# Optimization experiments

Measured on AMD Instinct MI355X. Metric: run time of the kernel, lower is better.

The kernel has to match this reference:

```python
import jax, jax.numpy as jnp
import numpy as np

B, C, H, W = 8, 256, 128, 128


def _bilinear_sample(img, gx, gy):
    """F.grid_sample(bilinear, padding_mode='zeros', align_corners=False).
    img: [B,C,H,W]; gx, gy: [B,H,W] normalized coords in [-1,1].
    Returns [B,C,H,W]."""
    Bi, Ci, Hi, Wi = img.shape
    ix = ((gx + 1.0) * Wi - 1.0) * 0.5  # pixel x coord
    iy = ((gy + 1.0) * Hi - 1.0) * 0.5  # pixel y coord
    ix0 = jnp.floor(ix)
    iy0 = jnp.floor(iy)
    wx1 = ix - ix0
    wy1 = iy - iy0
    bidx = jnp.arange(Bi)[:, None, None]

    def gather(iyf, ixf):
        valid = (ixf >= 0) & (ixf < Wi) & (iyf >= 0) & (iyf < Hi)
        iyc = jnp.clip(iyf, 0, Hi - 1).astype(jnp.int32)
        ixc = jnp.clip(ixf, 0, Wi - 1).astype(jnp.int32)
        v = img[bidx, :, iyc, ixc]  # [B,H,W,C]
        return jnp.where(valid[..., None], v, jnp.zeros((), img.dtype))

    v00 = gather(iy0, ix0)
    v01 = gather(iy0, ix0 + 1)
    v10 = gather(iy0 + 1, ix0)
    v11 = gather(iy0 + 1, ix0 + 1)
    w00 = ((1.0 - wy1) * (1.0 - wx1))[..., None]
    w01 = ((1.0 - wy1) * wx1)[..., None]
    w10 = (wy1 * (1.0 - wx1))[..., None]
    w11 = (wy1 * wx1)[..., None]
    out = v00 * w00 + v01 * w01 + v10 * w10 + v11 * w11  # [B,H,W,C]
    return out.transpose(0, 3, 1, 2)


def setup_inputs() -> dict:
    key = jax.random.key(0)
    ks = jax.random.split(key, 7)
    s = 1.0 / np.sqrt(C)
    return {
        "x": jax.random.normal(ks[0], (B, C, H, W), jnp.float32),
        "w_dw": jax.random.normal(ks[1], (C,), jnp.float32) * s,        # depthwise 1x1, no bias
        "w_off": jax.random.normal(ks[2], (2, C), jnp.float32) * s,     # offset 1x1 conv C->2
        "b_off": jax.random.normal(ks[3], (2,), jnp.float32) * 0.1,
        "w_pc": jax.random.normal(ks[4], (C, C), jnp.float32) * s,      # pointwise 1x1, no bias
        "w_W": jax.random.normal(ks[5], (C, C), jnp.float32) * s,       # residual-merge 1x1 conv
        "b_W": jax.random.normal(ks[6], (C,), jnp.float32) * 0.1,
    }


def reference(x, w_dw, w_off, b_off, w_pc, w_W, b_W):
    # offset = tanh(Conv1x1(x)) -> one shared (dx, dy) field (group == inplanes)
    offset = jnp.tanh(jnp.einsum('oc,bchw->bohw', w_off, x) + b_off[None, :, None, None])
    # depthwise 1x1 conv (bias=False) == per-channel scale
    dw = x * w_dw[None, :, None, None]
    # base normalized grid: X varies along W, Y along H (np.meshgrid convention)
    gx_base = jnp.linspace(-1.0, 1.0, W)[None, None, :]  # [1,1,W]
    gy_base = jnp.linspace(-1.0, 1.0, H)[None, :, None]  # [1,H,1]
    gx = jnp.clip(gx_base + offset[:, 0], -1.0, 1.0)  # [B,H,W]
    gy = jnp.clip(gy_base + offset[:, 1], -1.0, 1.0)
    sampled = _bilinear_sample(dw, gx, gy)             # [B,C,H,W]
    out = jnp.einsum('oc,bchw->bohw', w_pc, sampled)   # pointwise conv
    out = jnp.einsum('oc,bchw->bohw', w_W, out) + b_W[None, :, None, None]
    return out + x
```

## Files before the change

kernel.cpp:

```cpp
#include <hip/hip_runtime.h>
#include <hip/hip_bf16.h>

#define Bn 8
#define Cn 256
#define Hn 128
#define Wn 128
#define HWn (Hn * Wn)

typedef __attribute__((ext_vector_type(8))) short bfrag8;
typedef __attribute__((ext_vector_type(8))) unsigned short u16x8;
typedef __attribute__((ext_vector_type(4))) float f32x4;
typedef __attribute__((ext_vector_type(4))) unsigned int u32x4;

__device__ __forceinline__ float bf2f(unsigned short u) {
    unsigned int v = ((unsigned int)u) << 16;
    return __builtin_bit_cast(float, v);
}
__device__ __forceinline__ unsigned short f2bf(float f) {
    unsigned int u = __builtin_bit_cast(unsigned int, f);
    unsigned int lsb = (u >> 16) & 1u;
    u += 0x7fffu + lsb;
    return (unsigned short)(u >> 16);
}

__device__ __forceinline__ void load_lds16(const void* g, void* l) {
    __builtin_amdgcn_global_load_lds(
        (const __attribute__((address_space(1))) unsigned int*)g,
        (__attribute__((address_space(3))) unsigned int*)l,
        16, 0, 0);
}

__global__ __launch_bounds__(256)
void build_wcomb(const float* __restrict__ w_dw,
                 const float* __restrict__ w_pc,
                 const float* __restrict__ w_W,
                 unsigned short* __restrict__ wfrag) {
    const int o = blockIdx.x;
    const int c = threadIdx.x;
    float acc = 0.f;
#pragma unroll 8
    for (int k = 0; k < Cn; ++k)
        acc = fmaf(w_W[o * Cn + k], w_pc[k * Cn + c], acc);
    const int ob = o >> 4, lr = o & 15;
    const int ks = c >> 5, lg = (c & 31) >> 3, e = c & 7;
    const int lane = (lg << 4) + lr;
    wfrag[((((ob << 3) + ks) << 6) + lane) * 8 + e] = f2bf(acc * w_dw[c]);
}

__global__ __launch_bounds__(512, 2)
void prep_kernel(const float* __restrict__ x,
                 const float* __restrict__ w_off,
                 const float* __restrict__ b_off,
                 unsigned short* __restrict__ x_t,
                 float2* __restrict__ coords) {
    __shared__ __align__(16) char tile[256 * 256];
    __shared__ float wo[2][8][33];
    const int t = threadIdx.x;
    const int lane = t & 63;
    const int wv = t >> 6;
    int blk = blockIdx.x;
    blk = ((blk & 7) << 8) | (blk >> 3);
    const int b = blk >> 8;
    const int p0 = (blk & 255) << 6;
    const float* xp = x + ((size_t)b * Cn) * HWn + p0;

    {
        const int which = t >> 8, c = t & 255;
        wo[which][c >> 5][c & 31] = w_off[(which << 8) + c];
    }

    {
        const int r = lane >> 4;
        const int q = lane & 15;
#pragma unroll
        for (int i = 0; i < 8; ++i) {
            const int cbase = (wv << 5) + (i << 2);
            const int c = cbase + r;
            const int swz = (c ^ (c >> 4)) & 15;
            const float* src = xp + (size_t)c * HWn + ((q ^ swz) << 2);
            load_lds16(src, tile + (cbase << 8));
        }
    }
    __syncthreads();

    {
        const int pp = t >> 3;
        const int g = t & 7;
        float s0 = 0.f, s1 = 0.f;
        u16x8 res[4];
#pragma unroll
        for (int s = 0; s < 32; ++s) {
            const int c = (g << 5) + s;
            const int swz = (c ^ (c >> 4)) & 15;
            const int byte = (c << 8) + ((((pp >> 2) ^ swz)) << 4) + ((pp & 3) << 2);
            float v = *reinterpret_cast<const float*>(tile + byte);
            s0 = fmaf(v, wo[0][g][s], s0);
            s1 = fmaf(v, wo[1][g][s], s1);
            res[s >> 3][s & 7] = f2bf(v);
        }

        s0 += __shfl_xor(s0, 1); s0 += __shfl_xor(s0, 2); s0 += __shfl_xor(s0, 4);
        s1 += __shfl_xor(s1, 1); s1 += __shfl_xor(s1, 2); s1 += __shfl_xor(s1, 4);
        if (g == 0) {
            float o0 = tanhf(s0 + b_off[0]);
            float o1 = tanhf(s1 + b_off[1]);
            int p = p0 + pp;
            int yy = p >> 7, xx = p & 127;
            float gx = fminf(fmaxf(-1.f + xx * (2.f / 127.f) + o0, -1.f), 1.f);
            float gy = fminf(fmaxf(-1.f + yy * (2.f / 127.f) + o1, -1.f), 1.f);
            coords[(size_t)b * HWn + p] = make_float2(gx * 64.f + 63.5f, gy * 64.f + 63.5f);
        }

        unsigned short* dst = x_t + ((size_t)(b * HWn + p0 + pp)) * Cn + (g << 5);
#pragma unroll
        for (int j = 0; j < 4; ++j)
            *reinterpret_cast<u32x4*>(dst + (j << 3)) = __builtin_bit_cast(u32x4, res[j]);
    }
}

__global__ __launch_bounds__(512, 2)
void main_kernel(const float* __restrict__ x,
                 const float* __restrict__ b_W,
                 const unsigned short* __restrict__ x_t,
                 const float2* __restrict__ coords,
                 const unsigned short* __restrict__ wfrag,
                 float* __restrict__ out) {
    __shared__ __align__(16) char As[4][32 * 512];
    __shared__ __align__(16) float4 wts[32];
    const int t = threadIdx.x;
    const int lane = t & 63;
    const int wid = t >> 6;
    int blk = blockIdx.x;
    blk = ((blk & 7) << 9) | (blk >> 3);
    const int b = blk >> 9;
    const int p0 = (blk & 511) << 5;
    const size_t pixbase = (size_t)b * HWn + p0;
    const unsigned short* xtb = x_t + (size_t)b * HWn * Cn;

    if (t < 32) {
        float2 co = coords[pixbase + t];
        float ix = co.x, iy = co.y;
        float fx = floorf(ix), fy = floorf(iy);
        int ix0 = (int)fx, iy0 = (int)fy;
        float wx1 = ix - fx, wy1 = iy - fy;
        float wx0 = 1.f - wx1, wy0 = 1.f - wy1;
        bool vx0 = (ix0 >= 0) && (ix0 < Wn);
        bool vx1 = (ix0 >= -1) && (ix0 < Wn - 1);
        bool vy0 = (iy0 >= 0) && (iy0 < Hn);
        bool vy1 = (iy0 >= -1) && (iy0 < Hn - 1);
        float4 w;
        w.x = (vy0 && vx0) ? wy0 * wx0 : 0.f;
        w.y = (vy0 && vx1) ? wy0 * wx1 : 0.f;
        w.z = (vy1 && vx0) ? wy1 * wx0 : 0.f;
        w.w = (vy1 && vx1) ? wy1 * wx1 : 0.f;
        wts[t] = w;
    }

    {
        const int hp = lane >> 5;
        const int j = lane & 31;
        float2 co[2];
#pragma unroll
        for (int i = 0; i < 2; ++i)
            co[i] = coords[pixbase + (wid << 2) + (i << 1) + hp];

#pragma unroll
        for (int i = 0; i < 2; ++i) {
            const int p = (wid << 2) + (i << 1);
            const int px = p + hp;
            float ix = co[i].x, iy = co[i].y;
            int ix0 = (int)floorf(ix), iy0 = (int)floorf(iy);
            int cx0 = min(max(ix0, 0), Wn - 1), cx1 = min(max(ix0 + 1, 0), Wn - 1);
            int cy0 = min(max(iy0, 0), Hn - 1), cy1 = min(max(iy0 + 1, 0), Hn - 1);
            const int gch = (j ^ (px & 15)) << 3;
            const unsigned short* s00 = xtb + (size_t)(cy0 * Wn + cx0) * Cn + gch;
            const unsigned short* s01 = xtb + (size_t)(cy0 * Wn + cx1) * Cn + gch;
            const unsigned short* s10 = xtb + (size_t)(cy1 * Wn + cx0) * Cn + gch;
            const unsigned short* s11 = xtb + (size_t)(cy1 * Wn + cx1) * Cn + gch;
            load_lds16(s00, &As[0][p << 9]);
            load_lds16(s01, &As[1][p << 9]);
            load_lds16(s10, &As[2][p << 9]);
            load_lds16(s11, &As[3][p << 9]);
        }
    }
    __syncthreads();

    {
        const int px = t >> 4;
        const float4 w = wts[px];
#pragma unroll
        for (int q = 0; q < 2; ++q) {
            const int kc = (t & 15) + (q << 4);
            const int off = (px << 9) + ((kc ^ (px & 15)) << 4);
            u16x8 c00 = *reinterpret_cast<const u16x8*>(&As[0][off]);
            u16x8 c01 = *reinterpret_cast<const u16x8*>(&As[1][off]);
            u16x8 c10 = *reinterpret_cast<const u16x8*>(&As[2][off]);
            u16x8 c11 = *reinterpret_cast<const u16x8*>(&As[3][off]);
            u16x8 res;
#pragma unroll
            for (int e = 0; e < 8; ++e) {
                float r = w.x * bf2f(c00[e]) + w.y * bf2f(c01[e])
                        + w.z * bf2f(c10[e]) + w.w * bf2f(c11[e]);
                res[e] = f2bf(r);
            }
            *reinterpret_cast<u16x8*>(&As[0][off]) = res;
        }
    }
    __syncthreads();

    const int lr = lane & 15;
    const int lg = lane >> 4;
    f32x4 acc[2][2];
#pragma unroll
    for (int m = 0; m < 2; ++m)
#pragma unroll
        for (int n = 0; n < 2; ++n)
            acc[m][n] = (f32x4){0.f, 0.f, 0.f, 0.f};

#pragma unroll
    for (int ks = 0; ks < 8; ++ks) {
        bfrag8 a[2], bb[2];
        const int kc = (ks << 2) + lg;
#pragma unroll
        for (int n = 0; n < 2; ++n) {
            const int pr = (n << 4) + lr;
            const int off = (pr << 9) + ((kc ^ (pr & 15)) << 4);
            bb[n] = *reinterpret_cast<const bfrag8*>(&As[0][off]);
        }
#pragma unroll
        for (int m = 0; m < 2; ++m) {
            const int ob = (wid << 1) + m;
            const unsigned short* src = wfrag + ((((ob << 3) + ks) << 6) + lane) * 8;
            a[m] = *reinterpret_cast<const bfrag8*>(src);
        }
#pragma unroll
        for (int m = 0; m < 2; ++m)
#pragma unroll
            for (int n = 0; n < 2; ++n)
                acc[m][n] = __builtin_amdgcn_mfma_f32_16x16x32_bf16(a[m], bb[n], acc[m][n], 0, 0, 0);
    }

#pragma unroll
    for (int m = 0; m < 2; ++m) {
#pragma unroll
        for (int r = 0; r < 4; ++r) {
            int o = (wid << 5) + (m << 4) + (lg << 2) + r;
            float bw = b_W[o];
            size_t rowbase = ((size_t)b * Cn + o) * HWn + p0;
#pragma unroll
            for (int n = 0; n < 2; ++n) {
                size_t idx = rowbase + (n << 4) + lr;
                __builtin_nontemporal_store(acc[m][n][r] + bw + x[idx], &out[idx]);
            }
        }
    }
}

extern "C" void kernel_launch(void* const* d_in, const int* in_sizes, int n_in,
                              void* d_out, int out_size, void* d_ws, size_t ws_size,
                              hipStream_t stream) {
    const float* x     = (const float*)d_in[0];
    const float* w_dw  = (const float*)d_in[1];
    const float* w_off = (const float*)d_in[2];
    const float* b_off = (const float*)d_in[3];
    const float* w_pc  = (const float*)d_in[4];
    const float* w_W   = (const float*)d_in[5];
    const float* b_W   = (const float*)d_in[6];
    float* out = (float*)d_out;

    char* ws = (char*)d_ws;
    unsigned short* x_t   = (unsigned short*)ws;
    float2* coords        = (float2*)(ws + 67108864);
    unsigned short* wcomb = (unsigned short*)(ws + 67108864 + 1048576);

    build_wcomb<<<dim3(256), dim3(256), 0, stream>>>(w_dw, w_pc, w_W, wcomb);
    prep_kernel<<<dim3(2048), dim3(512), 0, stream>>>(x, w_off, b_off, x_t, coords);
    main_kernel<<<dim3(4096), dim3(512), 0, stream>>>(x, b_W, x_t, coords, wcomb, out);
}
```

Measured before the change: 121.3 us.

## Restructure prep kernel into double-buffered channel-slice pipeline over 512 pixels

The prep kernel now has each block handle 512 pixels, with one pixel per thread, and walks the 256 channels in eight 32-channel slices. Slice loads go into two LDS buffers so the next slice's global-to-LDS copy overlaps the current slice's offset-conv accumulation and bf16 transpose store. This removes the shuffle reduction and the swizzled tile reads. In exchange the grid shrinks from 2048 to 256 blocks with one block per CU, which may leave CUs underused and lower the memory parallelism available to this bandwidth-bound step.

```diff
diff --git a/kernel.cpp b/kernel.cpp
--- a/kernel.cpp
+++ b/kernel.cpp
@@ -47,75 +47,70 @@
     wfrag[((((ob << 3) + ks) << 6) + lane) * 8 + e] = f2bf(acc * w_dw[c]);
 }
 
-__global__ __launch_bounds__(512, 2)
+__global__ __launch_bounds__(512, 1)
 void prep_kernel(const float* __restrict__ x,
                  const float* __restrict__ w_off,
                  const float* __restrict__ b_off,
                  unsigned short* __restrict__ x_t,
                  float2* __restrict__ coords) {
-    __shared__ __align__(16) char tile[256 * 256];
-    __shared__ float wo[2][8][33];
+    __shared__ __align__(16) char bufs[2][32 * 512 * 4];
+    __shared__ float wo[2][256];
     const int t = threadIdx.x;
     const int lane = t & 63;
     const int wv = t >> 6;
     int blk = blockIdx.x;
-    blk = ((blk & 7) << 8) | (blk >> 3);
-    const int b = blk >> 8;
-    const int p0 = (blk & 255) << 6;
+    blk = ((blk & 7) << 5) | (blk >> 3);
+    const int b = blk >> 5;
+    const int p0 = (blk & 31) << 9;
     const float* xp = x + ((size_t)b * Cn) * HWn + p0;
 
-    {
-        const int which = t >> 8, c = t & 255;
-        wo[which][c >> 5][c & 31] = w_off[(which << 8) + c];
-    }
-
-    {
-        const int r = lane >> 4;
-        const int q = lane & 15;
-#pragma unroll
-        for (int i = 0; i < 8; ++i) {
-            const int cbase = (wv << 5) + (i << 2);
-            const int c = cbase + r;
-            const int swz = (c ^ (c >> 4)) & 15;
-            const float* src = xp + (size_t)c * HWn + ((q ^ swz) << 2);
-            load_lds16(src, tile + (cbase << 8));
-        }
-    }
-    __syncthreads();
-
-    {
-        const int pp = t >> 3;
-        const int g = t & 7;
-        float s0 = 0.f, s1 = 0.f;
+    wo[t >> 8][t & 255] = w_off[t];
+
+    float s0 = 0.f, s1 = 0.f;
+
+    auto dma = [&](int sl, char* buf) {
+#pragma unroll
+        for (int i = 0; i < 4; ++i) {
+            const int cl = (wv << 2) + i;
+            const float* src = xp + (size_t)((sl << 5) + cl) * HWn + (lane << 2);
+            load_lds16(src,       buf + (cl << 11));
+            load_lds16(src + 256, buf + (cl << 11) + 1024);
+        }
+    };
+
+    auto conv = [&](int sl, const char* buf) {
+        const float* bf = (const float*)buf;
         u16x8 res[4];
 #pragma unroll
         for (int s = 0; s < 32; ++s) {
-            const int c = (g << 5) + s;
-            const int swz = (c ^ (c >> 4)) & 15;
-            const int byte = (c << 8) + ((((pp >> 2) ^ swz)) << 4) + ((pp & 3) << 2);
-            float v = *reinterpret_cast<const float*>(tile + byte);
-            s0 = fmaf(v, wo[0][g][s], s0);
-            s1 = fmaf(v, wo[1][g][s], s1);
+            float v = bf[(s << 9) + t];
+            s0 = fmaf(v, wo[0][(sl << 5) + s], s0);
+            s1 = fmaf(v, wo[1][(sl << 5) + s], s1);
             res[s >> 3][s & 7] = f2bf(v);
         }
-
-        s0 += __shfl_xor(s0, 1); s0 += __shfl_xor(s0, 2); s0 += __shfl_xor(s0, 4);
-        s1 += __shfl_xor(s1, 1); s1 += __shfl_xor(s1, 2); s1 += __shfl_xor(s1, 4);
-        if (g == 0) {
-            float o0 = tanhf(s0 + b_off[0]);
-            float o1 = tanhf(s1 + b_off[1]);
-            int p = p0 + pp;
-            int yy = p >> 7, xx = p & 127;
-            float gx = fminf(fmaxf(-1.f + xx * (2.f / 127.f) + o0, -1.f), 1.f);
-            float gy = fminf(fmaxf(-1.f + yy * (2.f / 127.f) + o1, -1.f), 1.f);
-            coords[(size_t)b * HWn + p] = make_float2(gx * 64.f + 63.5f, gy * 64.f + 63.5f);
-        }
-
-        unsigned short* dst = x_t + ((size_t)(b * HWn + p0 + pp)) * Cn + (g << 5);
+        unsigned short* dst = x_t + ((size_t)(b * HWn + p0 + t)) * Cn + (sl << 5);
 #pragma unroll
         for (int j = 0; j < 4; ++j)
             *reinterpret_cast<u32x4*>(dst + (j << 3)) = __builtin_bit_cast(u32x4, res[j]);
-    }
+    };
+
+    dma(0, bufs[0]);
+    __syncthreads();
+#pragma unroll
+    for (int sl = 1; sl < 8; ++sl) {
+        dma(sl, bufs[sl & 1]);
+        conv(sl - 1, bufs[(sl - 1) & 1]);
+        __syncthreads();
+    }
+    conv(7, bufs[1]);
+
+    float o0 = tanhf(s0 + b_off[0]);
+    float o1 = tanhf(s1 + b_off[1]);
+    int p = p0 + t;
+    int yy = p >> 7, xx = p & 127;
+    float gx = fminf(fmaxf(-1.f + xx * (2.f / 127.f) + o0, -1.f), 1.f);
+    float gy = fminf(fmaxf(-1.f + yy * (2.f / 127.f) + o1, -1.f), 1.f);
+    coords[(size_t)b * HWn + p] = make_float2(gx * 64.f + 63.5f, gy * 64.f + 63.5f);
 }
 
 __global__ __launch_bounds__(512, 2)
@@ -274,6 +269,6 @@
     unsigned short* wcomb = (unsigned short*)(ws + 67108864 + 1048576);
 
     build_wcomb<<<dim3(256), dim3(256), 0, stream>>>(w_dw, w_pc, w_W, wcomb);
-    prep_kernel<<<dim3(2048), dim3(512), 0, stream>>>(x, w_off, b_off, x_t, coords);
+    prep_kernel<<<dim3(256), dim3(512), 0, stream>>>(x, w_off, b_off, x_t, coords);
     main_kernel<<<dim3(4096), dim3(512), 0, stream>>>(x, b_W, x_t, coords, wcomb, out);
 }
```

New measurement: 118.2 us. 2.5% less time.
